# Kernel tuning notes

Hardware: AMD Instinct MI355X
Metric: run time of the kernel (lower is better)

Reference implementation:

```python
import jax, jax.numpy as jnp
import numpy as np

T, IN, H, OUT = 4096, 2048, 2048, 1


def setup_inputs() -> dict:
    key = jax.random.key(0)
    ks = jax.random.split(key, 7)
    s = 0.02  # small init scale to keep gates in a sane range
    return {
        "x": jax.random.normal(ks[0], (T, 1, IN), dtype=jnp.float32),
        "W_ih": s * jax.random.normal(ks[1], (4 * H, IN), dtype=jnp.float32),
        "W_hh": s * jax.random.normal(ks[2], (4 * H, H), dtype=jnp.float32),
        "b_ih": s * jax.random.normal(ks[3], (4 * H,), dtype=jnp.float32),
        "b_hh": s * jax.random.normal(ks[4], (4 * H,), dtype=jnp.float32),
        "W_out": s * jax.random.normal(ks[5], (OUT, H), dtype=jnp.float32),
        "b_out": s * jax.random.normal(ks[6], (OUT,), dtype=jnp.float32),
    }


def reference(x, W_ih, W_hh, b_ih, b_hh, W_out, b_out):
    # Faithful LSTMCell loop (PyTorch gate order i, f, g, o) + per-step Linear.
    hidden = W_hh.shape[1]

    def step(carry, x_t):  # x_t: [1, IN]
        h, c = carry
        gates = x_t @ W_ih.T + b_ih + h @ W_hh.T + b_hh  # [1, 4H]
        i, f, g, o = jnp.split(gates, 4, axis=-1)
        i = jax.nn.sigmoid(i)
        f = jax.nn.sigmoid(f)
        g = jnp.tanh(g)
        o = jax.nn.sigmoid(o)
        c = f * c + i * g
        h = o * jnp.tanh(c)
        y = (h @ W_out.T + b_out)[0, 0]  # scalar, output_size == 1
        return (h, c), y

    h0 = jnp.zeros((1, hidden), dtype=x.dtype)
    c0 = jnp.zeros((1, hidden), dtype=x.dtype)
    _, res = jax.lax.scan(step, (h0, c0), x)
    return res  # [T]
```

## Files before the change

### kernel.cpp

```cpp
#include <hip/hip_runtime.h>

#define T_STEPS 4096
#define HD 2048
#define G4 8192
#define NWG 256
#define NTH 1024
#define SENT 0x7FC0DEADu
#define SMEM_BYTES (131072 + 8192 + 128)

typedef __attribute__((ext_vector_type(8))) short bf16x8;
typedef __attribute__((ext_vector_type(4))) float f32x4;
typedef __attribute__((ext_vector_type(2))) float f32x2;
typedef __attribute__((ext_vector_type(8))) unsigned short u16x8;

static __device__ __forceinline__ unsigned short f2bf(float f){
  union { float f; unsigned int u; } v; v.f = f;
  unsigned int r = (v.u + 0x7fffu + ((v.u >> 16) & 1u)) >> 16;
  return (unsigned short)r;
}
static __device__ __forceinline__ float bf2f(unsigned short s){
  union { unsigned int u; float f; } v; v.u = ((unsigned int)s) << 16;
  return v.f;
}
static __device__ __forceinline__ float blo(unsigned int u){
  return __uint_as_float(u << 16);
}
static __device__ __forceinline__ float bhi(unsigned int u){
  return __uint_as_float(u & 0xffff0000u);
}

static __device__ __forceinline__ f32x2 ld2_uc(const float* p){
  f32x2 r;
  asm volatile("global_load_dwordx2 %0, %1, off sc0 sc1\n\ts_waitcnt vmcnt(0)"
               : "=v"(r) : "v"(p) : "memory");
  return r;
}
static __device__ __forceinline__ void st_uc(float* p, float v){
  asm volatile("global_store_dword %0, %1, off sc0 sc1" :: "v"(p), "v"(v) : "memory");
}

__global__ void init_kernel(const float* __restrict__ b_ih, const float* __restrict__ b_hh,
                            float* __restrict__ bias, float* __restrict__ Hbuf){
  int i = blockIdx.x*blockDim.x + threadIdx.x;
  int stride = gridDim.x*blockDim.x;
  const int NTOT = G4 + (T_STEPS+1)*HD;
  union { unsigned int u; float f; } sent; sent.u = SENT;
  for (int idx = i; idx < NTOT; idx += stride){
    if (idx < G4) bias[idx] = b_ih[idx] + b_hh[idx];
    else {
      int j = idx - G4;
      Hbuf[j] = (j < HD) ? 0.f : sent.f;
    }
  }
}

__global__ __launch_bounds__(256) void gemm_xp(const float* __restrict__ X,
                                               const float* __restrict__ W,
                                               const float* __restrict__ bias,
                                               unsigned short* __restrict__ XP){
  __shared__ __align__(16) unsigned short As[128][40];
  __shared__ __align__(16) unsigned short Bs[128][40];
  const int tid = threadIdx.x;
  const int bx = blockIdx.x & 63;
  const int by = blockIdx.x >> 6;
  const int row0 = by*128, col0 = bx*128;
  const int l = tid & 63, w = tid >> 6;
  const int wrow = (w>>1)*64, wcol = (w&1)*64;
  const int lr = l & 15, lk = l >> 4;

  f32x4 acc[4][4];
  #pragma unroll
  for (int mi=0; mi<4; mi++)
    #pragma unroll
    for (int ni=0; ni<4; ni++)
      acc[mi][ni] = (f32x4){0.f,0.f,0.f,0.f};

  const int sr = tid >> 1;
  const int sh = (tid & 1) * 16;
  const float* xb = X + (size_t)(row0+sr)*2048 + sh;
  const float* wb = W + (size_t)(col0+sr)*2048 + sh;

  for (int k0 = 0; k0 < 2048; k0 += 32){
    __syncthreads();
    u16x8 va[2], vb[2];
    #pragma unroll
    for (int q=0; q<2; q++){
      float4 u = *(const float4*)(xb + k0 + q*8);
      float4 v = *(const float4*)(xb + k0 + q*8 + 4);
      u16x8 t;
      t[0]=f2bf(u.x); t[1]=f2bf(u.y); t[2]=f2bf(u.z); t[3]=f2bf(u.w);
      t[4]=f2bf(v.x); t[5]=f2bf(v.y); t[6]=f2bf(v.z); t[7]=f2bf(v.w);
      va[q]=t;
      float4 p = *(const float4*)(wb + k0 + q*8);
      float4 r = *(const float4*)(wb + k0 + q*8 + 4);
      u16x8 s;
      s[0]=f2bf(p.x); s[1]=f2bf(p.y); s[2]=f2bf(p.z); s[3]=f2bf(p.w);
      s[4]=f2bf(r.x); s[5]=f2bf(r.y); s[6]=f2bf(r.z); s[7]=f2bf(r.w);
      vb[q]=s;
    }
    *(u16x8*)&As[sr][sh]   = va[0];
    *(u16x8*)&As[sr][sh+8] = va[1];
    *(u16x8*)&Bs[sr][sh]   = vb[0];
    *(u16x8*)&Bs[sr][sh+8] = vb[1];
    __syncthreads();

    bf16x8 af[4], bfr[4];
    #pragma unroll
    for (int mi=0; mi<4; mi++) af[mi]  = *(const bf16x8*)&As[wrow+mi*16+lr][lk*8];
    #pragma unroll
    for (int ni=0; ni<4; ni++) bfr[ni] = *(const bf16x8*)&Bs[wcol+ni*16+lr][lk*8];
    #pragma unroll
    for (int mi=0; mi<4; mi++)
      #pragma unroll
      for (int ni=0; ni<4; ni++)
        acc[mi][ni] = __builtin_amdgcn_mfma_f32_16x16x32_bf16(af[mi], bfr[ni], acc[mi][ni], 0,0,0);
  }

  #pragma unroll
  for (int ni=0; ni<4; ni++){
    const int jc = col0 + wcol + ni*16 + lr;
    const float bv = bias[jc];
    #pragma unroll
    for (int mi=0; mi<4; mi++){
      const int tr0 = row0 + wrow + mi*16 + lk*4;
      #pragma unroll
      for (int r=0; r<4; r++)
        XP[(size_t)(tr0+r)*G4 + jc] = f2bf(acc[mi][ni][r] + bv);
    }
  }
}

__global__ __launch_bounds__(NTH, 4) void recur(const unsigned short* __restrict__ XP,
                                                const float* __restrict__ Whh,
                                                float* __restrict__ Hbuf){
  extern __shared__ char smem[];
  float* h_lds = (float*)(smem + 131072);
  float* gsum  = (float*)(smem + 131072 + 8192);
  const int g = blockIdx.x;
  const int tid = threadIdx.x;
  const int l = tid & 63, w = tid >> 6;

  #pragma unroll
  for (int ri=0; ri<2; ri++){
    const int rr = 2*w + ri;
    const size_t jrow = (size_t)(rr>>3)*HD + (size_t)g*8 + (rr&7);
    const float* wp = Whh + jrow*HD + l*4;
    #pragma unroll
    for (int cp=0; cp<4; cp++){
      float4 fa = *(const float4*)(wp + (2*cp)*256);
      float4 fb = *(const float4*)(wp + (2*cp+1)*256);
      uint4 pk;
      pk.x = ((unsigned)f2bf(fa.y)<<16) | f2bf(fa.x);
      pk.y = ((unsigned)f2bf(fa.w)<<16) | f2bf(fa.z);
      pk.z = ((unsigned)f2bf(fb.y)<<16) | f2bf(fb.x);
      pk.w = ((unsigned)f2bf(fb.w)<<16) | f2bf(fb.z);
      *(uint4*)(smem + (size_t)((ri*4+cp)*1024 + tid)*16) = pk;
    }
  }

  float c_reg = 0.f;
  float xpv[4] = {0,0,0,0};

  for (int t=0; t<T_STEPS; ++t){
    if (tid < 8){
      #pragma unroll
      for (int q=0; q<4; q++)
        xpv[q] = bf2f(XP[(size_t)t*G4 + (size_t)q*HD + g*8 + tid]);
    }
    const float* hp = Hbuf + (size_t)t*HD + tid*2;
    f32x2 hv;
    do {
      hv = ld2_uc(hp);
    } while (__float_as_uint(hv[0]) == SENT || __float_as_uint(hv[1]) == SENT);
    *(f32x2*)&h_lds[tid*2] = hv;
    __syncthreads();

    float a0 = 0.f, a1 = 0.f;
    #pragma unroll
    for (int cp=0; cp<4; cp++){
      float4 ha = *(const float4*)&h_lds[(2*cp)*256 + l*4];
      float4 hb = *(const float4*)&h_lds[(2*cp+1)*256 + l*4];
      uint4 w0 = *(const uint4*)(smem + (size_t)((cp  )*1024 + tid)*16);
      uint4 w1 = *(const uint4*)(smem + (size_t)((4+cp)*1024 + tid)*16);
      a0 += blo(w0.x)*ha.x + bhi(w0.x)*ha.y + blo(w0.y)*ha.z + bhi(w0.y)*ha.w
          + blo(w0.z)*hb.x + bhi(w0.z)*hb.y + blo(w0.w)*hb.z + bhi(w0.w)*hb.w;
      a1 += blo(w1.x)*ha.x + bhi(w1.x)*ha.y + blo(w1.y)*ha.z + bhi(w1.y)*ha.w
          + blo(w1.z)*hb.x + bhi(w1.z)*hb.y + blo(w1.w)*hb.z + bhi(w1.w)*hb.w;
    }
    #pragma unroll
    for (int off=32; off; off>>=1){
      a0 += __shfl_xor(a0, off, 64);
      a1 += __shfl_xor(a1, off, 64);
    }
    if (l == 0){ gsum[2*w] = a0; gsum[2*w+1] = a1; }
    __syncthreads();

    if (tid < 8){
      float ipre = gsum[tid]    + xpv[0];
      float fpre = gsum[8+tid]  + xpv[1];
      float gpre = gsum[16+tid] + xpv[2];
      float opre = gsum[24+tid] + xpv[3];
      float iv = 1.f/(1.f + __expf(-ipre));
      float fv = 1.f/(1.f + __expf(-fpre));
      float e2 = __expf(-2.f*gpre);
      float gv = (1.f - e2)/(1.f + e2);
      float ov = 1.f/(1.f + __expf(-opre));
      c_reg = fv*c_reg + iv*gv;
      float e2c = __expf(-2.f*c_reg);
      float th = (1.f - e2c)/(1.f + e2c);
      st_uc(Hbuf + (size_t)(t+1)*HD + g*8 + tid, ov*th);
    }
  }
}

__global__ __launch_bounds__(256) void out_gemv(const float* __restrict__ Hbuf,
                                                const float* __restrict__ Wout,
                                                const float* __restrict__ bout,
                                                float* __restrict__ y){
  const int t = blockIdx.x;
  const int tid = threadIdx.x;
  const float* h = Hbuf + (size_t)(t+1)*HD;
  float4 a0 = *(const float4*)(h + tid*8);
  float4 a1 = *(const float4*)(h + tid*8 + 4);
  float4 w0 = *(const float4*)(Wout + tid*8);
  float4 w1 = *(const float4*)(Wout + tid*8 + 4);
  float s = a0.x*w0.x + a0.y*w0.y + a0.z*w0.z + a0.w*w0.w
          + a1.x*w1.x + a1.y*w1.y + a1.z*w1.z + a1.w*w1.w;
  #pragma unroll
  for (int off=32; off; off>>=1) s += __shfl_xor(s, off, 64);
  __shared__ float ps[4];
  if ((tid & 63) == 0) ps[tid>>6] = s;
  __syncthreads();
  if (tid == 0) y[t] = ps[0]+ps[1]+ps[2]+ps[3] + bout[0];
}

extern "C" void kernel_launch(void* const* d_in, const int* in_sizes, int n_in,
                              void* d_out, int out_size, void* d_ws, size_t ws_size,
                              hipStream_t stream) {
  const float* x    = (const float*)d_in[0];
  const float* Wih  = (const float*)d_in[1];
  const float* Whh  = (const float*)d_in[2];
  const float* b_ih = (const float*)d_in[3];
  const float* b_hh = (const float*)d_in[4];
  const float* Wout = (const float*)d_in[5];
  const float* bout = (const float*)d_in[6];
  float* y = (float*)d_out;

  char* ws = (char*)d_ws;
  unsigned short* XP = (unsigned short*)(ws);
  float* Hbuf        = (float*)(ws + 67108864);
  float* bias        = (float*)(ws + 100671488);

  init_kernel<<<2048, 256, 0, stream>>>(b_ih, b_hh, bias, Hbuf);
  gemm_xp<<<2048, 256, 0, stream>>>(x, Wih, bias, XP);

  hipFuncSetAttribute((const void*)recur,
                      hipFuncAttributeMaxDynamicSharedMemorySize, SMEM_BYTES);
  void* args[] = {(void*)&XP, (void*)&Whh, (void*)&Hbuf};
  hipLaunchCooperativeKernel((void*)recur, dim3(NWG), dim3(NTH), args,
                             SMEM_BYTES, stream);

  out_gemv<<<T_STEPS, 256, 0, stream>>>(Hbuf, Wout, bout, y);
}
```

Before: 11.90 ms.

## Use MFMA for recurrent matvec and exchange hidden state as bf16

The per-step recurrent h·W_hh product moves from scalar FMAs with wave shuffles to bf16 MFMA 16x16x32 instructions, with weights relaid out in LDS as MFMA B fragments and h broadcast as the A fragment. The global hidden-state exchange buffer changes from fp32 to bf16 with a bf16 NaN sentinel, which halves polling and store traffic on the latency-bound cross-workgroup handoff. The h LDS buffer is double-buffered by step parity, and the reduction goes through a partial-sum array read by one wave. Hidden state is now rounded to bf16 every step, which adds precision loss that accumulates over the recurrence.

```diff
diff --git a/kernel.cpp b/kernel.cpp
--- a/kernel.cpp
+++ b/kernel.cpp
@@ -5,12 +5,15 @@
 #define G4 8192
 #define NWG 256
 #define NTH 1024
-#define SENT 0x7FC0DEADu
-#define SMEM_BYTES (131072 + 8192 + 128)
+#define HSENT 0xFF80u
+#define HSENT2 0xFF80FF80u
+
+#define HB_OFF  131072
+#define P_OFF   (131072 + 8192)
+#define SMEM_BYTES (131072 + 8192 + 2048)
 
 typedef __attribute__((ext_vector_type(8))) short bf16x8;
 typedef __attribute__((ext_vector_type(4))) float f32x4;
-typedef __attribute__((ext_vector_type(2))) float f32x2;
 typedef __attribute__((ext_vector_type(8))) unsigned short u16x8;
 
 static __device__ __forceinline__ unsigned short f2bf(float f){
@@ -22,34 +25,28 @@
   union { unsigned int u; float f; } v; v.u = ((unsigned int)s) << 16;
   return v.f;
 }
-static __device__ __forceinline__ float blo(unsigned int u){
-  return __uint_as_float(u << 16);
-}
-static __device__ __forceinline__ float bhi(unsigned int u){
-  return __uint_as_float(u & 0xffff0000u);
-}
-
-static __device__ __forceinline__ f32x2 ld2_uc(const float* p){
-  f32x2 r;
-  asm volatile("global_load_dwordx2 %0, %1, off sc0 sc1\n\ts_waitcnt vmcnt(0)"
+
+static __device__ __forceinline__ unsigned int ld1_uc(const unsigned int* p){
+  unsigned int r;
+  asm volatile("global_load_dword %0, %1, off sc0 sc1\n\ts_waitcnt vmcnt(0)"
                : "=v"(r) : "v"(p) : "memory");
   return r;
 }
-static __device__ __forceinline__ void st_uc(float* p, float v){
-  asm volatile("global_store_dword %0, %1, off sc0 sc1" :: "v"(p), "v"(v) : "memory");
+static __device__ __forceinline__ void st2_uc(unsigned short* p, unsigned int v){
+  asm volatile("global_store_short %0, %1, off sc0 sc1" :: "v"(p), "v"(v) : "memory");
 }
 
 __global__ void init_kernel(const float* __restrict__ b_ih, const float* __restrict__ b_hh,
-                            float* __restrict__ bias, float* __restrict__ Hbuf){
+                            float* __restrict__ bias, unsigned int* __restrict__ Hb32){
   int i = blockIdx.x*blockDim.x + threadIdx.x;
   int stride = gridDim.x*blockDim.x;
-  const int NTOT = G4 + (T_STEPS+1)*HD;
-  union { unsigned int u; float f; } sent; sent.u = SENT;
+  const int HB_U32 = (T_STEPS+1)*HD/2;
+  const int NTOT = G4 + HB_U32;
   for (int idx = i; idx < NTOT; idx += stride){
     if (idx < G4) bias[idx] = b_ih[idx] + b_hh[idx];
     else {
       int j = idx - G4;
-      Hbuf[j] = (j < HD) ? 0.f : sent.f;
+      Hb32[j] = (j < HD/2) ? 0u : HSENT2;
     }
   }
 }
@@ -132,100 +129,116 @@
 
 __global__ __launch_bounds__(NTH, 4) void recur(const unsigned short* __restrict__ XP,
                                                 const float* __restrict__ Whh,
-                                                float* __restrict__ Hbuf){
+                                                unsigned short* __restrict__ Hbuf){
   extern __shared__ char smem[];
-  float* h_lds = (float*)(smem + 131072);
-  float* gsum  = (float*)(smem + 131072 + 8192);
+  float* part = (float*)(smem + P_OFF);
   const int g = blockIdx.x;
   const int tid = threadIdx.x;
   const int l = tid & 63, w = tid >> 6;
 
   #pragma unroll
-  for (int ri=0; ri<2; ri++){
-    const int rr = 2*w + ri;
-    const size_t jrow = (size_t)(rr>>3)*HD + (size_t)g*8 + (rr&7);
-    const float* wp = Whh + jrow*HD + l*4;
-    #pragma unroll
-    for (int cp=0; cp<4; cp++){
-      float4 fa = *(const float4*)(wp + (2*cp)*256);
-      float4 fb = *(const float4*)(wp + (2*cp+1)*256);
+  for (int n=0; n<2; n++)
+    #pragma unroll
+    for (int kt=0; kt<4; kt++){
+      const int rr = n*16 + (l & 15);
+      const size_t jrow = (size_t)(rr>>3)*HD + (size_t)g*8 + (rr&7);
+      const int k = w*128 + kt*32 + (l>>4)*8;
+      const float* wp = Whh + jrow*HD + k;
+      float4 fa = *(const float4*)wp;
+      float4 fb = *(const float4*)(wp + 4);
       uint4 pk;
       pk.x = ((unsigned)f2bf(fa.y)<<16) | f2bf(fa.x);
       pk.y = ((unsigned)f2bf(fa.w)<<16) | f2bf(fa.z);
       pk.z = ((unsigned)f2bf(fb.y)<<16) | f2bf(fb.x);
       pk.w = ((unsigned)f2bf(fb.w)<<16) | f2bf(fb.z);
-      *(uint4*)(smem + (size_t)((ri*4+cp)*1024 + tid)*16) = pk;
-    }
-  }
+      *(uint4*)(smem + (size_t)(((w*8 + n*4 + kt)*64 + l)*16)) = pk;
+    }
+  __syncthreads();
 
   float c_reg = 0.f;
-  float xpv[4] = {0,0,0,0};
 
   for (int t=0; t<T_STEPS; ++t){
+    float xpv0=0.f, xpv1=0.f, xpv2=0.f, xpv3=0.f;
     if (tid < 8){
+      const unsigned short* xp = XP + (size_t)t*G4 + (size_t)g*8 + tid;
+      xpv0 = bf2f(xp[0]);
+      xpv1 = bf2f(xp[HD]);
+      xpv2 = bf2f(xp[2*HD]);
+      xpv3 = bf2f(xp[3*HD]);
+    }
+    bf16x8 bfr0[4], bfr1[4];
+    #pragma unroll
+    for (int kt=0; kt<4; kt++){
+      bfr0[kt] = *(const bf16x8*)(smem + (size_t)(((w*8 +      kt)*64 + l)*16));
+      bfr1[kt] = *(const bf16x8*)(smem + (size_t)(((w*8 + 4 + kt)*64 + l)*16));
+    }
+
+    unsigned int hv;
+    {
+      const unsigned int* hp = (const unsigned int*)(Hbuf + (size_t)t*HD) + tid;
+      do { hv = ld1_uc(hp); }
+      while ((hv & 0xFFFFu) == HSENT || (hv >> 16) == HSENT);
+    }
+    unsigned int* hdst = (unsigned int*)(smem + HB_OFF + (t&1)*4096);
+    hdst[tid] = hv;
+    __syncthreads();
+
+    const char* hb = smem + HB_OFF + (t&1)*4096;
+    bf16x8 af[4];
+    #pragma unroll
+    for (int kt=0; kt<4; kt++)
+      af[kt] = *(const bf16x8*)(hb + (w*256 + kt*64 + (l>>4)*16));
+
+    f32x4 acc0 = (f32x4){0.f,0.f,0.f,0.f};
+    f32x4 acc1 = (f32x4){0.f,0.f,0.f,0.f};
+    #pragma unroll
+    for (int kt=0; kt<4; kt++){
+      acc0 = __builtin_amdgcn_mfma_f32_16x16x32_bf16(af[kt], bfr0[kt], acc0, 0,0,0);
+      acc1 = __builtin_amdgcn_mfma_f32_16x16x32_bf16(af[kt], bfr1[kt], acc1, 0,0,0);
+    }
+    if (l < 16){
+      part[w*32 + l]      = acc0[0];
+      part[w*32 + 16 + l] = acc1[0];
+    }
+    __syncthreads();
+
+    if (w == 0 && l < 32){
+      float tot = 0.f;
       #pragma unroll
-      for (int q=0; q<4; q++)
-        xpv[q] = bf2f(XP[(size_t)t*G4 + (size_t)q*HD + g*8 + tid]);
-    }
-    const float* hp = Hbuf + (size_t)t*HD + tid*2;
-    f32x2 hv;
-    do {
-      hv = ld2_uc(hp);
-    } while (__float_as_uint(hv[0]) == SENT || __float_as_uint(hv[1]) == SENT);
-    *(f32x2*)&h_lds[tid*2] = hv;
-    __syncthreads();
-
-    float a0 = 0.f, a1 = 0.f;
-    #pragma unroll
-    for (int cp=0; cp<4; cp++){
-      float4 ha = *(const float4*)&h_lds[(2*cp)*256 + l*4];
-      float4 hb = *(const float4*)&h_lds[(2*cp+1)*256 + l*4];
-      uint4 w0 = *(const uint4*)(smem + (size_t)((cp  )*1024 + tid)*16);
-      uint4 w1 = *(const uint4*)(smem + (size_t)((4+cp)*1024 + tid)*16);
-      a0 += blo(w0.x)*ha.x + bhi(w0.x)*ha.y + blo(w0.y)*ha.z + bhi(w0.y)*ha.w
-          + blo(w0.z)*hb.x + bhi(w0.z)*hb.y + blo(w0.w)*hb.z + bhi(w0.w)*hb.w;
-      a1 += blo(w1.x)*ha.x + bhi(w1.x)*ha.y + blo(w1.y)*ha.z + bhi(w1.y)*ha.w
-          + blo(w1.z)*hb.x + bhi(w1.z)*hb.y + blo(w1.w)*hb.z + bhi(w1.w)*hb.w;
-    }
-    #pragma unroll
-    for (int off=32; off; off>>=1){
-      a0 += __shfl_xor(a0, off, 64);
-      a1 += __shfl_xor(a1, off, 64);
-    }
-    if (l == 0){ gsum[2*w] = a0; gsum[2*w+1] = a1; }
-    __syncthreads();
-
-    if (tid < 8){
-      float ipre = gsum[tid]    + xpv[0];
-      float fpre = gsum[8+tid]  + xpv[1];
-      float gpre = gsum[16+tid] + xpv[2];
-      float opre = gsum[24+tid] + xpv[3];
-      float iv = 1.f/(1.f + __expf(-ipre));
-      float fv = 1.f/(1.f + __expf(-fpre));
-      float e2 = __expf(-2.f*gpre);
-      float gv = (1.f - e2)/(1.f + e2);
-      float ov = 1.f/(1.f + __expf(-opre));
-      c_reg = fv*c_reg + iv*gv;
-      float e2c = __expf(-2.f*c_reg);
-      float th = (1.f - e2c)/(1.f + e2c);
-      st_uc(Hbuf + (size_t)(t+1)*HD + g*8 + tid, ov*th);
-    }
-  }
-}
-
-__global__ __launch_bounds__(256) void out_gemv(const float* __restrict__ Hbuf,
+      for (int q=0; q<16; q++) tot += part[q*32 + l];
+      float fg = __shfl_down(tot, 8, 64);
+      float gg = __shfl_down(tot, 16, 64);
+      float og = __shfl_down(tot, 24, 64);
+      if (l < 8){
+        float ipre = tot + xpv0;
+        float fpre = fg  + xpv1;
+        float gpre = gg  + xpv2;
+        float opre = og  + xpv3;
+        float iv = 1.f/(1.f + __expf(-ipre));
+        float fv = 1.f/(1.f + __expf(-fpre));
+        float e2 = __expf(-2.f*gpre);
+        float gv = (1.f - e2)/(1.f + e2);
+        float ov = 1.f/(1.f + __expf(-opre));
+        c_reg = fv*c_reg + iv*gv;
+        float e2c = __expf(-2.f*c_reg);
+        float th = (1.f - e2c)/(1.f + e2c);
+        st2_uc(Hbuf + (size_t)(t+1)*HD + (size_t)g*8 + l, (unsigned int)f2bf(ov*th));
+      }
+    }
+  }
+}
+
+__global__ __launch_bounds__(256) void out_gemv(const unsigned short* __restrict__ Hbuf,
                                                 const float* __restrict__ Wout,
                                                 const float* __restrict__ bout,
                                                 float* __restrict__ y){
   const int t = blockIdx.x;
   const int tid = threadIdx.x;
-  const float* h = Hbuf + (size_t)(t+1)*HD;
-  float4 a0 = *(const float4*)(h + tid*8);
-  float4 a1 = *(const float4*)(h + tid*8 + 4);
+  u16x8 hv = *(const u16x8*)(Hbuf + (size_t)(t+1)*HD + tid*8);
   float4 w0 = *(const float4*)(Wout + tid*8);
   float4 w1 = *(const float4*)(Wout + tid*8 + 4);
-  float s = a0.x*w0.x + a0.y*w0.y + a0.z*w0.z + a0.w*w0.w
-          + a1.x*w1.x + a1.y*w1.y + a1.z*w1.z + a1.w*w1.w;
+  float s = bf2f(hv[0])*w0.x + bf2f(hv[1])*w0.y + bf2f(hv[2])*w0.z + bf2f(hv[3])*w0.w
+          + bf2f(hv[4])*w1.x + bf2f(hv[5])*w1.y + bf2f(hv[6])*w1.z + bf2f(hv[7])*w1.w;
   #pragma unroll
   for (int off=32; off; off>>=1) s += __shfl_xor(s, off, 64);
   __shared__ float ps[4];
@@ -247,11 +260,11 @@
   float* y = (float*)d_out;
 
   char* ws = (char*)d_ws;
-  unsigned short* XP = (unsigned short*)(ws);
-  float* Hbuf        = (float*)(ws + 67108864);
-  float* bias        = (float*)(ws + 100671488);
-
-  init_kernel<<<2048, 256, 0, stream>>>(b_ih, b_hh, bias, Hbuf);
+  unsigned short* XP   = (unsigned short*)(ws);
+  unsigned short* Hbuf = (unsigned short*)(ws + 67108864);
+  float* bias          = (float*)(ws + 83890176);
+
+  init_kernel<<<2048, 256, 0, stream>>>(b_ih, b_hh, bias, (unsigned int*)Hbuf);
   gemm_xp<<<2048, 256, 0, stream>>>(x, Wih, bias, XP);
 
   hipFuncSetAttribute((const void*)recur,
```

Result: faster. 10.75 ms (-9.7%).
